# Kernel tuning notes

Hardware: AMD Instinct MI355X
Metric: run time of the kernel (lower is better)

The kernel has to match this reference:

```python
import jax, jax.numpy as jnp
import numpy as np

B, N_COLS, N_PROMPTS, D = 1024, 256, 128, 256


def _ln(x, g, b, eps=1e-5):
    m = jnp.mean(x, axis=-1, keepdims=True)
    v = jnp.mean(jnp.square(x - m), axis=-1, keepdims=True)
    return (x - m) * jax.lax.rsqrt(v + eps) * g + b


def setup_inputs() -> dict:
    key = jax.random.key(0)
    ks = jax.random.split(key, 10)
    d_rs = D ** -0.5
    return {
        "x": jax.random.normal(ks[0], (B, N_COLS), jnp.float32),
        "prev_cell_out": jax.random.normal(ks[1], (B, N_PROMPTS, D), jnp.float32),
        "feature_emb_weight": jax.random.uniform(ks[2], (N_COLS, D), jnp.float32, -d_rs, d_rs),
        "feature_emb_bias": jax.random.uniform(ks[3], (N_COLS, D), jnp.float32, -d_rs, d_rs),
        "ln_emb_g": jnp.ones((D,), jnp.float32),
        "ln_emb_b": jnp.zeros((D,), jnp.float32),
        "ln_col_g": jnp.ones((D,), jnp.float32),
        "ln_col_b": jnp.zeros((D,), jnp.float32),
        "ln_prompt_g": jnp.ones((D,), jnp.float32),
        "ln_prompt_b": jnp.zeros((D,), jnp.float32),
        # torch Linear(2*D, D): weight [D, 2*D], y = x @ W^T + b
        "dense_imp_w": jax.random.normal(ks[4], (D, 2 * D), jnp.float32) * (2 * D) ** -0.5,
        "dense_imp_b": jnp.zeros((D,), jnp.float32),
        "emb_column": jax.random.normal(ks[5], (N_COLS, D), jnp.float32) * 0.01,
        "emb_prompt": jax.random.normal(ks[6], (N_PROMPTS, D), jnp.float32) * 0.01,
        # dense_expand = Linear(1, n_prompts): weight [n_prompts,1] squeezed -> [n_prompts]
        "expand_w": jax.random.normal(ks[7], (N_PROMPTS,), jnp.float32),
        "expand_b": jax.random.normal(ks[8], (N_PROMPTS,), jnp.float32) * 0.01,
    }


def reference(x, prev_cell_out, feature_emb_weight, feature_emb_bias,
              ln_emb_g, ln_emb_b, ln_col_g, ln_col_b, ln_prompt_g, ln_prompt_b,
              dense_imp_w, dense_imp_b, emb_column, emb_prompt,
              expand_w, expand_b):
    # feature embedding: [B, N, D]
    x_emb = jax.nn.relu(jnp.einsum('bn,nd->bnd', x, feature_emb_weight) + feature_emb_bias)
    x_emb = _ln(x_emb, ln_emb_g, ln_emb_b)
    # prompt update with residual
    xp = jnp.broadcast_to(emb_prompt[None], (x.shape[0], N_PROMPTS, D))  # [B, P, D]
    cat = jnp.concatenate([_ln(xp, ln_prompt_g, ln_prompt_b), prev_cell_out], axis=-1)  # [B, P, 2D]
    xp = jnp.einsum('bpk,dk->bpd', cat, dense_imp_w) + dense_imp_b + xp
    # column keys (shared across batch)
    col = _ln(emb_column, ln_col_g, ln_col_b)  # [N, D]
    mask = jax.nn.softmax(jnp.einsum('bpd,nd->bpn', xp, col), axis=-1)  # [B, P, N]
    V = jnp.einsum('bpn,bnd->bpd', mask, x_emb)  # [B, P, D]
    return V * (1.0 + expand_w)[None, :, None] + expand_b[None, :, None]
```

## Files before the change

kernel.cpp:

```cpp
#include <hip/hip_runtime.h>

#define NCOLS 256
#define NP    128
#define DD    256

typedef _Float16 half2 __attribute__((ext_vector_type(2)));
typedef _Float16 half4 __attribute__((ext_vector_type(4)));
typedef float    f32x4 __attribute__((ext_vector_type(4)));

#define MFMA16(a,b,c) __builtin_amdgcn_mfma_f32_16x16x16f16(a,b,c,0,0,0)

#define WS_COL_LN   0
#define WS_LNP      262144
#define WS_BASE     393216
#define WS_BLOG     524288
#define WS_CW16     655360
#define WS_WB16     786432

#define LDS_CWP   3072
#define LDS_XE0   68608
#define LDS_XE1   101376
#define SMEM_MAIN 134144


__global__ __launch_bounds__(256) void k0a(
    const float* __restrict__ emb_column, const float* __restrict__ emb_prompt,
    const float* __restrict__ ln_col_g, const float* __restrict__ ln_col_b,
    const float* __restrict__ ln_prompt_g, const float* __restrict__ ln_prompt_b,
    const float* __restrict__ few, const float* __restrict__ feb,
    char* __restrict__ ws)
{
    __shared__ float red[10];
    int blk = blockIdx.x, tid = threadIdx.x;
    if (blk < 384) {
        const float *src, *g, *bb; float* dst;
        if (blk < 256) { int r = blk;     src = emb_column + r*DD; g = ln_col_g;    bb = ln_col_b;    dst = (float*)(ws + WS_COL_LN) + r*DD; }
        else           { int r = blk-256; src = emb_prompt + r*DD; g = ln_prompt_g; bb = ln_prompt_b; dst = (float*)(ws + WS_LNP) + r*DD; }
        float v = src[tid];
        float s = v, q = v*v;
        #pragma unroll
        for (int off = 32; off; off >>= 1) { s += __shfl_xor(s, off); q += __shfl_xor(q, off); }
        int wid = tid >> 6, lane = tid & 63;
        if (lane == 0) { red[wid] = s; red[4+wid] = q; }
        __syncthreads();
        if (tid == 0) {
            float S = red[0]+red[1]+red[2]+red[3];
            float Q = red[4]+red[5]+red[6]+red[7];
            float mu = S * (1.0f/DD);
            float var = Q * (1.0f/DD) - mu*mu;
            red[8] = mu; red[9] = rsqrtf(var + 1e-5f);
        }
        __syncthreads();
        dst[tid] = (v - red[8]) * red[9] * g[tid] + bb[tid];
    } else {
        int base = (blk - 384) * 512;
        half2* wb = (half2*)(ws + WS_WB16);
        #pragma unroll
        for (int j = 0; j < 2; ++j) {
            int idx = base + j*256 + tid;
            half2 h; h[0] = (_Float16)few[idx]; h[1] = (_Float16)feb[idx];
            wb[idx] = h;
        }
    }
}

__global__ __launch_bounds__(256) void k0b(
    const float* __restrict__ diw, const float* __restrict__ dib,
    const float* __restrict__ emb_prompt, char* __restrict__ ws)
{
    __shared__ float rowv[DD];
    int blk = blockIdx.x, tid = threadIdx.x;
    if (blk < 256) {
        int n = blk;
        const float* col_ln = (const float*)(ws + WS_COL_LN);
        rowv[tid] = col_ln[n*DD + tid];
        __syncthreads();
        float acc = 0.f;
        #pragma unroll 4
        for (int d = 0; d < DD; ++d) acc += rowv[d] * diw[d*512 + 256 + tid];
        int nt = n >> 4, lr = n & 15;
        int kc = tid >> 4, lq = (tid >> 2) & 3, j = tid & 3;
        ((_Float16*)(ws + WS_CW16))[((kc*16 + nt)*64 + lq*16 + lr)*4 + j] = (_Float16)acc;
    } else {
        int p = blk - 256;
        const float* lnp = (const float*)(ws + WS_LNP);
        rowv[tid] = lnp[p*DD + tid];
        __syncthreads();
        float acc = 0.f;
        #pragma unroll 4
        for (int k = 0; k < DD; ++k) acc += rowv[k] * diw[tid*512 + k];
        ((float*)(ws + WS_BASE))[p*DD + tid] = acc + dib[tid] + emb_prompt[p*DD + tid];
    }
}

__global__ __launch_bounds__(256) void k0c(char* __restrict__ ws)
{
    __shared__ float bs[DD];
    int p = blockIdx.x, n = threadIdx.x;
    const float* base   = (const float*)(ws + WS_BASE);
    const float* col_ln = (const float*)(ws + WS_COL_LN);
    bs[n] = base[p*DD + n];
    __syncthreads();
    float acc = 0.f;
    #pragma unroll 4
    for (int d = 0; d < DD; ++d) acc += bs[d] * col_ln[n*DD + d];
    ((float*)(ws + WS_BLOG))[p*DD + n] = acc;
}

__global__ __launch_bounds__(1024) void trompt_main(
    const float* __restrict__ x, const float* __restrict__ prev,
    const float* __restrict__ expand_w, const float* __restrict__ expand_b,
    const float* __restrict__ ln_emb_g, const float* __restrict__ ln_emb_b,
    const char* __restrict__ ws, float* __restrict__ out)
{
    extern __shared__ char smem[];
    float* x_s  = (float*)(smem);
    float* sm_m = (float*)(smem + 1024);
    float* sm_l = (float*)(smem + 2048);
    char*  cwP  = smem + LDS_CWP;
    char*  xe0  = smem + LDS_XE0;
    char*  xe1  = smem + LDS_XE1;

    const char*  cwbase = ws + WS_CW16;
    const half2* WB     = (const half2*)(ws + WS_WB16);

    int b = blockIdx.x;
    int tid = threadIdx.x;
    int w = tid >> 6, l = tid & 63, lq = l >> 4, lr = l & 15;
    int pt = w >> 1, h = w & 1;
    int p  = 16*pt + lr;
    int pswz = (p & 7) << 4;

    if (tid < 256) x_s[tid] = x[b*NCOLS + tid];

    #pragma unroll
    for (int i = 0; i < 8; ++i) {
        int u = tid + 1024*i;
        *(uint4*)(cwP + u*16) = *(const uint4*)(cwbase + u*16);
    }

    half4 pfrag[16];
    {
        const float* prow = prev + ((size_t)b*NP + p)*DD + 4*lq;
        #pragma unroll
        for (int kc = 0; kc < 16; ++kc) {
            f32x4 v = *(const f32x4*)(prow + 16*kc);
            half4 hh;
            #pragma unroll
            for (int j = 0; j < 4; ++j) hh[j] = (_Float16)v[j];
            pfrag[kc] = hh;
        }
    }

    f32x4 acc[8];
    {
        const float* blrow = (const float*)(ws + WS_BLOG) + (size_t)p*DD + 4*lq;
        #pragma unroll
        for (int a = 0; a < 8; ++a) acc[a] = *(const f32x4*)(blrow + 16*(8*h + a));
    }

    __syncthreads();

    {
        const char* cwl = cwP + l*8 + (size_t)(8*h)*512;
        #pragma unroll
        for (int kc = 0; kc < 16; ++kc) {
            const char* fb = cwl + (size_t)kc*8192;
            half4 bp = pfrag[kc];
            #pragma unroll
            for (int a = 0; a < 8; ++a)
                acc[a] = MFMA16(*(const half4*)(fb + a*512), bp, acc[a]);
        }
    }

    float pmax = -1e30f;
    #pragma unroll
    for (int a = 0; a < 8; ++a)
        #pragma unroll
        for (int r = 0; r < 4; ++r) pmax = fmaxf(pmax, acc[a][r]);
    pmax = fmaxf(pmax, __shfl_xor(pmax, 16));
    pmax = fmaxf(pmax, __shfl_xor(pmax, 32));
    if (lq == 0) sm_m[h*128 + p] = pmax;
    __syncthreads();
    float m = fmaxf(pmax, sm_m[(1 ^ h)*128 + p]);

    float s = 0.f;
    #pragma unroll
    for (int a = 0; a < 8; ++a)
        #pragma unroll
        for (int r = 0; r < 4; ++r) { float e = __expf(acc[a][r] - m); acc[a][r] = e; s += e; }
    s += __shfl_xor(s, 16);
    s += __shfl_xor(s, 32);
    if (lq == 0) sm_l[h*128 + p] = s;
    __syncthreads();
    float inv = 1.0f / (s + sm_l[(1 ^ h)*128 + p]);

    #pragma unroll
    for (int a = 0; a < 8; ++a) {
        int nb = (8*h + a)*32 + lq*8;
        half4 hh;
        #pragma unroll
        for (int r = 0; r < 4; ++r) hh[r] = (_Float16)(acc[a][r] * inv);
        *(half4*)(cwP + p*512 + (nb ^ pswz)) = hh;
    }

    float gcc[4], bcc[4];
    #pragma unroll
    for (int cc = 0; cc < 4; ++cc) {
        gcc[cc] = ln_emb_g[l + 64*cc];
        bcc[cc] = ln_emb_b[l + 64*cc];
    }

    auto compute_xe = [&](int c, char* xebuf) {
        int kc2w = w >> 2, lq2 = w & 3;
        float vj[4][4];
        #pragma unroll
        for (int j = 0; j < 4; ++j) {
            int n = c*64 + 16*kc2w + 4*lq2 + j;
            float xv = x_s[n];
            const half2* wbrow = WB + n*DD;
            float ss = 0.f, qq = 0.f;
            #pragma unroll
            for (int cc = 0; cc < 4; ++cc) {
                half2 pp = wbrow[l + 64*cc];
                float e = fmaf(xv, (float)pp[0], (float)pp[1]);
                e = e > 0.f ? e : 0.f;
                vj[j][cc] = e; ss += e; qq += e*e;
            }
            #pragma unroll
            for (int off = 32; off; off >>= 1) { ss += __shfl_xor(ss, off); qq += __shfl_xor(qq, off); }
            float mu = ss * (1.0f/DD);
            float rs = rsqrtf(qq*(1.0f/DD) - mu*mu + 1e-5f);
            #pragma unroll
            for (int cc = 0; cc < 4; ++cc)
                vj[j][cc] = (vj[j][cc]-mu)*rs*gcc[cc] + bcc[cc];
        }
        #pragma unroll
        for (int cc = 0; cc < 4; ++cc) {
            int dt = 4*cc + (l >> 4);
            half4 hh;
            #pragma unroll
            for (int j = 0; j < 4; ++j) hh[j] = (_Float16)vj[j][cc];
            *(half4*)(xebuf + (((kc2w*16 + dt)*64) + lq2*16 + lr)*8) = hh;
        }
    };

    compute_xe(0, xe0);

    f32x4 acc_v[8];
    #pragma unroll
    for (int dtl = 0; dtl < 8; ++dtl) acc_v[dtl] = (f32x4){0.f,0.f,0.f,0.f};

    __syncthreads();

    for (int c = 0; c < 4; ++c) {
        char* xec = (c & 1) ? xe1 : xe0;
        char* xen = (c & 1) ? xe0 : xe1;

        half4 bp[4];
        #pragma unroll
        for (int kc2 = 0; kc2 < 4; ++kc2)
            bp[kc2] = *(const half4*)(cwP + p*512 + ((c*128 + kc2*32 + lq*8) ^ pswz));

        if (c < 3) compute_xe(c+1, xen);

        const char* xel = xec + l*8;
        #pragma unroll
        for (int kc2 = 0; kc2 < 4; ++kc2) {
            const char* xb = xel + (size_t)(kc2*16 + 8*h)*512;
            half4 bpc = bp[kc2];
            #pragma unroll
            for (int dtl = 0; dtl < 8; ++dtl)
                acc_v[dtl] = MFMA16(*(const half4*)(xb + dtl*512), bpc, acc_v[dtl]);
        }

        if (c < 3) __syncthreads();
    }

    {
        float sw = 1.0f + expand_w[p];
        float sb = expand_b[p];
        float* orow = out + ((size_t)b*NP + p)*DD + 128*h + 4*lq;
        #pragma unroll
        for (int dtl = 0; dtl < 8; ++dtl) {
            f32x4 v = acc_v[dtl];
            #pragma unroll
            for (int r = 0; r < 4; ++r) v[r] = v[r]*sw + sb;
            *(f32x4*)(orow + 16*dtl) = v;
        }
    }
}

extern "C" void kernel_launch(void* const* d_in, const int* in_sizes, int n_in,
                              void* d_out, int out_size, void* d_ws, size_t ws_size,
                              hipStream_t stream) {
    (void)in_sizes; (void)n_in; (void)out_size; (void)ws_size;
    const float* x           = (const float*)d_in[0];
    const float* prev        = (const float*)d_in[1];
    const float* few         = (const float*)d_in[2];
    const float* feb         = (const float*)d_in[3];
    const float* ln_emb_g    = (const float*)d_in[4];
    const float* ln_emb_b    = (const float*)d_in[5];
    const float* ln_col_g    = (const float*)d_in[6];
    const float* ln_col_b    = (const float*)d_in[7];
    const float* ln_prompt_g = (const float*)d_in[8];
    const float* ln_prompt_b = (const float*)d_in[9];
    const float* diw         = (const float*)d_in[10];
    const float* dib         = (const float*)d_in[11];
    const float* emb_column  = (const float*)d_in[12];
    const float* emb_prompt  = (const float*)d_in[13];
    const float* expand_w    = (const float*)d_in[14];
    const float* expand_b    = (const float*)d_in[15];
    char* ws = (char*)d_ws;
    float* out = (float*)d_out;

    k0a<<<512, 256, 0, stream>>>(emb_column, emb_prompt, ln_col_g, ln_col_b,
                                 ln_prompt_g, ln_prompt_b, few, feb, ws);
    k0b<<<384, 256, 0, stream>>>(diw, dib, emb_prompt, ws);
    k0c<<<128, 256, 0, stream>>>(ws);

    (void)hipFuncSetAttribute(reinterpret_cast<const void*>(trompt_main),
                              hipFuncAttributeMaxDynamicSharedMemorySize, SMEM_MAIN);
    trompt_main<<<1024, 1024, SMEM_MAIN, stream>>>(x, prev, expand_w, expand_b,
                                                   ln_emb_g, ln_emb_b, ws, out);
}
```

Before: 195.5 us.

## Split prompts across two blocks and stream column weights through double-buffered LDS

```diff
diff --git a/kernel.cpp b/kernel.cpp
--- a/kernel.cpp
+++ b/kernel.cpp
@@ -17,10 +17,11 @@
 #define WS_CW16     655360
 #define WS_WB16     786432
 
-#define LDS_CWP   3072
-#define LDS_XE0   68608
-#define LDS_XE1   101376
-#define SMEM_MAIN 134144
+#define LDS_CW0   2048
+#define LDS_CW1   34816
+#define LDS_XEA   34816
+#define LDS_XEB   51200
+#define SMEM_MAIN 67584
 
 
 __global__ __launch_bounds__(256) void k0a(
@@ -107,7 +108,7 @@
     ((float*)(ws + WS_BLOG))[p*DD + n] = acc;
 }
 
-__global__ __launch_bounds__(1024) void trompt_main(
+__global__ __launch_bounds__(512, 4) void trompt_main(
     const float* __restrict__ x, const float* __restrict__ prev,
     const float* __restrict__ expand_w, const float* __restrict__ expand_b,
     const float* __restrict__ ln_emb_g, const float* __restrict__ ln_emb_b,
@@ -116,28 +117,26 @@
     extern __shared__ char smem[];
     float* x_s  = (float*)(smem);
     float* sm_m = (float*)(smem + 1024);
-    float* sm_l = (float*)(smem + 2048);
-    char*  cwP  = smem + LDS_CWP;
-    char*  xe0  = smem + LDS_XE0;
-    char*  xe1  = smem + LDS_XE1;
+    float* sm_l = (float*)(smem + 1536);
+    char*  cw0  = smem + LDS_CW0;
+    char*  cw1  = smem + LDS_CW1;
+    char*  Pb   = smem + LDS_CW0;
+    char*  xeA  = smem + LDS_XEA;
+    char*  xeB  = smem + LDS_XEB;
 
     const char*  cwbase = ws + WS_CW16;
     const half2* WB     = (const half2*)(ws + WS_WB16);
 
-    int b = blockIdx.x;
+    int bid = blockIdx.x;
+    int b = bid >> 1, ph = bid & 1;
     int tid = threadIdx.x;
     int w = tid >> 6, l = tid & 63, lq = l >> 4, lr = l & 15;
     int pt = w >> 1, h = w & 1;
-    int p  = 16*pt + lr;
-    int pswz = (p & 7) << 4;
+    int pl = 16*pt + lr;
+    int p  = 64*ph + pl;
+    int pswz = (pl & 7) << 4;
 
     if (tid < 256) x_s[tid] = x[b*NCOLS + tid];
-
-    #pragma unroll
-    for (int i = 0; i < 8; ++i) {
-        int u = tid + 1024*i;
-        *(uint4*)(cwP + u*16) = *(const uint4*)(cwbase + u*16);
-    }
 
     half4 pfrag[16];
     {
@@ -156,21 +155,57 @@
     {
         const float* blrow = (const float*)(ws + WS_BLOG) + (size_t)p*DD + 4*lq;
         #pragma unroll
-        for (int a = 0; a < 8; ++a) acc[a] = *(const f32x4*)(blrow + 16*(8*h + a));
-    }
-
-    __syncthreads();
-
-    {
-        const char* cwl = cwP + l*8 + (size_t)(8*h)*512;
+        for (int a = 0; a < 8; ++a)
+            acc[a] = *(const f32x4*)(blrow + 16*(4*(a>>1) + 2*h + (a&1)));
+    }
+
+    auto stage_cw = [&](int c, char* dst) {
+        #pragma unroll
+        for (int i = 0; i < 4; ++i) {
+            int u = tid + 512*i;
+            int kc = u >> 7, ntg = (u >> 5) & 3, rem = u & 31;
+            uint4 v = *(const uint4*)(cwbase + kc*8192 + c*2048 + ntg*512 + rem*16);
+            *(uint4*)(dst + u*16) = v;
+        }
+    };
+
+    stage_cw(0, cw0);
+    __syncthreads();
+
+    #pragma unroll
+    for (int c = 0; c < 4; ++c) {
+        char* cwc = (c & 1) ? cw1 : cw0;
+        char* cwn = (c & 1) ? cw0 : cw1;
+
+        uint4 st[4];
+        if (c < 3) {
+            #pragma unroll
+            for (int i = 0; i < 4; ++i) {
+                int u = tid + 512*i;
+                int kc = u >> 7, ntg = (u >> 5) & 3, rem = u & 31;
+                st[i] = *(const uint4*)(cwbase + kc*8192 + (c+1)*2048 + ntg*512 + rem*16);
+            }
+        }
+
+        const char* cwl = cwc + l*8 + h*1024;
         #pragma unroll
         for (int kc = 0; kc < 16; ++kc) {
-            const char* fb = cwl + (size_t)kc*8192;
+            const char* fb = cwl + kc*2048;
+            half4 a0 = *(const half4*)(fb);
+            half4 a1 = *(const half4*)(fb + 512);
             half4 bp = pfrag[kc];
-            #pragma unroll
-            for (int a = 0; a < 8; ++a)
-                acc[a] = MFMA16(*(const half4*)(fb + a*512), bp, acc[a]);
-        }
+            acc[2*c]   = MFMA16(a0, bp, acc[2*c]);
+            acc[2*c+1] = MFMA16(a1, bp, acc[2*c+1]);
+        }
+
+        if (c < 3) {
+            #pragma unroll
+            for (int i = 0; i < 4; ++i) {
+                int u = tid + 512*i;
+                *(uint4*)(cwn + u*16) = st[i];
+            }
+        }
+        __syncthreads();
     }
 
     float pmax = -1e30f;
@@ -180,9 +215,9 @@
         for (int r = 0; r < 4; ++r) pmax = fmaxf(pmax, acc[a][r]);
     pmax = fmaxf(pmax, __shfl_xor(pmax, 16));
     pmax = fmaxf(pmax, __shfl_xor(pmax, 32));
-    if (lq == 0) sm_m[h*128 + p] = pmax;
-    __syncthreads();
-    float m = fmaxf(pmax, sm_m[(1 ^ h)*128 + p]);
+    if (lq == 0) sm_m[h*64 + pl] = pmax;
+    __syncthreads();
+    float m = fmaxf(pmax, sm_m[(1 ^ h)*64 + pl]);
 
     float s = 0.f;
     #pragma unroll
@@ -191,17 +226,17 @@
         for (int r = 0; r < 4; ++r) { float e = __expf(acc[a][r] - m); acc[a][r] = e; s += e; }
     s += __shfl_xor(s, 16);
     s += __shfl_xor(s, 32);
-    if (lq == 0) sm_l[h*128 + p] = s;
-    __syncthreads();
-    float inv = 1.0f / (s + sm_l[(1 ^ h)*128 + p]);
+    if (lq == 0) sm_l[h*64 + pl] = s;
+    __syncthreads();
+    float inv = 1.0f / (s + sm_l[(1 ^ h)*64 + pl]);
 
     #pragma unroll
     for (int a = 0; a < 8; ++a) {
-        int nb = (8*h + a)*32 + lq*8;
+        int nb = (4*(a>>1) + 2*h + (a&1))*32 + lq*8;
         half4 hh;
         #pragma unroll
         for (int r = 0; r < 4; ++r) hh[r] = (_Float16)(acc[a][r] * inv);
-        *(half4*)(cwP + p*512 + (nb ^ pswz)) = hh;
+        *(half4*)(Pb + pl*512 + (nb ^ pswz)) = hh;
     }
 
     float gcc[4], bcc[4];
@@ -211,41 +246,41 @@
         bcc[cc] = ln_emb_b[l + 64*cc];
     }
 
-    auto compute_xe = [&](int c, char* xebuf) {
+    auto compute_xe = [&](int cc, char* xebuf) {
         int kc2w = w >> 2, lq2 = w & 3;
         float vj[4][4];
         #pragma unroll
         for (int j = 0; j < 4; ++j) {
-            int n = c*64 + 16*kc2w + 4*lq2 + j;
+            int n = cc*32 + 16*kc2w + 4*lq2 + j;
             float xv = x_s[n];
             const half2* wbrow = WB + n*DD;
             float ss = 0.f, qq = 0.f;
             #pragma unroll
-            for (int cc = 0; cc < 4; ++cc) {
-                half2 pp = wbrow[l + 64*cc];
+            for (int ccc = 0; ccc < 4; ++ccc) {
+                half2 pp = wbrow[l + 64*ccc];
                 float e = fmaf(xv, (float)pp[0], (float)pp[1]);
                 e = e > 0.f ? e : 0.f;
-                vj[j][cc] = e; ss += e; qq += e*e;
+                vj[j][ccc] = e; ss += e; qq += e*e;
             }
             #pragma unroll
             for (int off = 32; off; off >>= 1) { ss += __shfl_xor(ss, off); qq += __shfl_xor(qq, off); }
             float mu = ss * (1.0f/DD);
             float rs = rsqrtf(qq*(1.0f/DD) - mu*mu + 1e-5f);
             #pragma unroll
-            for (int cc = 0; cc < 4; ++cc)
-                vj[j][cc] = (vj[j][cc]-mu)*rs*gcc[cc] + bcc[cc];
-        }
-        #pragma unroll
-        for (int cc = 0; cc < 4; ++cc) {
-            int dt = 4*cc + (l >> 4);
+            for (int ccc = 0; ccc < 4; ++ccc)
+                vj[j][ccc] = (vj[j][ccc]-mu)*rs*gcc[ccc] + bcc[ccc];
+        }
+        #pragma unroll
+        for (int ccc = 0; ccc < 4; ++ccc) {
+            int dt = 4*ccc + (l >> 4);
             half4 hh;
             #pragma unroll
-            for (int j = 0; j < 4; ++j) hh[j] = (_Float16)vj[j][cc];
+            for (int j = 0; j < 4; ++j) hh[j] = (_Float16)vj[j][ccc];
             *(half4*)(xebuf + (((kc2w*16 + dt)*64) + lq2*16 + lr)*8) = hh;
         }
     };
 
-    compute_xe(0, xe0);
+    compute_xe(0, xeA);
 
     f32x4 acc_v[8];
     #pragma unroll
@@ -253,28 +288,24 @@
 
     __syncthreads();
 
-    for (int c = 0; c < 4; ++c) {
-        char* xec = (c & 1) ? xe1 : xe0;
-        char* xen = (c & 1) ? xe0 : xe1;
-
-        half4 bp[4];
-        #pragma unroll
-        for (int kc2 = 0; kc2 < 4; ++kc2)
-            bp[kc2] = *(const half4*)(cwP + p*512 + ((c*128 + kc2*32 + lq*8) ^ pswz));
-
-        if (c < 3) compute_xe(c+1, xen);
+    for (int cc = 0; cc < 8; ++cc) {
+        char* xec = (cc & 1) ? xeB : xeA;
+        char* xen = (cc & 1) ? xeA : xeB;
+
+        half4 bp0 = *(const half4*)(Pb + pl*512 + ((cc*64 +  0 + lq*8) ^ pswz));
+        half4 bp1 = *(const half4*)(Pb + pl*512 + ((cc*64 + 32 + lq*8) ^ pswz));
+
+        if (cc < 7) compute_xe(cc+1, xen);
 
         const char* xel = xec + l*8;
         #pragma unroll
-        for (int kc2 = 0; kc2 < 4; ++kc2) {
-            const char* xb = xel + (size_t)(kc2*16 + 8*h)*512;
-            half4 bpc = bp[kc2];
-            #pragma unroll
-            for (int dtl = 0; dtl < 8; ++dtl)
-                acc_v[dtl] = MFMA16(*(const half4*)(xb + dtl*512), bpc, acc_v[dtl]);
-        }
-
-        if (c < 3) __syncthreads();
+        for (int dtl = 0; dtl < 8; ++dtl)
+            acc_v[dtl] = MFMA16(*(const half4*)(xel + (size_t)(8*h + dtl)*512), bp0, acc_v[dtl]);
+        #pragma unroll
+        for (int dtl = 0; dtl < 8; ++dtl)
+            acc_v[dtl] = MFMA16(*(const half4*)(xel + (size_t)(16 + 8*h + dtl)*512), bp1, acc_v[dtl]);
+
+        __syncthreads();
     }
 
     {
@@ -321,6 +352,6 @@
 
     (void)hipFuncSetAttribute(reinterpret_cast<const void*>(trompt_main),
                               hipFuncAttributeMaxDynamicSharedMemorySize, SMEM_MAIN);
-    trompt_main<<<1024, 1024, SMEM_MAIN, stream>>>(x, prev, expand_w, expand_b,
-                                                   ln_emb_g, ln_emb_b, ws, out);
-}
+    trompt_main<<<2048, 512, SMEM_MAIN, stream>>>(x, prev, expand_w, expand_b,
+                                                  ln_emb_g, ln_emb_b, ws, out);
+}
```

After: 223.3 us. +14.2%, slower.

## Use 16x16x32 f16 MFMA for logits and merge softmax into one barrier

Applied to the files above, without the earlier changes.

```diff
diff --git a/kernel.cpp b/kernel.cpp
--- a/kernel.cpp
+++ b/kernel.cpp
@@ -6,9 +6,11 @@
 
 typedef _Float16 half2 __attribute__((ext_vector_type(2)));
 typedef _Float16 half4 __attribute__((ext_vector_type(4)));
+typedef _Float16 half8 __attribute__((ext_vector_type(8)));
 typedef float    f32x4 __attribute__((ext_vector_type(4)));
 
 #define MFMA16(a,b,c) __builtin_amdgcn_mfma_f32_16x16x16f16(a,b,c,0,0,0)
+#define MFMA32(a,b,c) __builtin_amdgcn_mfma_f32_16x16x32_f16(a,b,c,0,0,0)
 
 #define WS_COL_LN   0
 #define WS_LNP      262144
@@ -79,8 +81,8 @@
         #pragma unroll 4
         for (int d = 0; d < DD; ++d) acc += rowv[d] * diw[d*512 + 256 + tid];
         int nt = n >> 4, lr = n & 15;
-        int kc = tid >> 4, lq = (tid >> 2) & 3, j = tid & 3;
-        ((_Float16*)(ws + WS_CW16))[((kc*16 + nt)*64 + lq*16 + lr)*4 + j] = (_Float16)acc;
+        int kc32 = tid >> 5, lq = (tid >> 3) & 3, jj = tid & 7;
+        ((_Float16*)(ws + WS_CW16))[(kc32*16 + nt)*512 + (lq*16 + lr)*8 + jj] = (_Float16)acc;
     } else {
         int p = blk - 256;
         const float* lnp = (const float*)(ws + WS_LNP);
@@ -133,74 +135,77 @@
 
     if (tid < 256) x_s[tid] = x[b*NCOLS + tid];
 
+    half8 pf[8];
+    {
+        const float* prow = prev + ((size_t)b*NP + p)*DD + 8*lq;
+        #pragma unroll
+        for (int kc = 0; kc < 8; ++kc) {
+            f32x4 v0 = *(const f32x4*)(prow + 32*kc);
+            f32x4 v1 = *(const f32x4*)(prow + 32*kc + 4);
+            half8 hh;
+            #pragma unroll
+            for (int j = 0; j < 4; ++j) { hh[j] = (_Float16)v0[j]; hh[4+j] = (_Float16)v1[j]; }
+            pf[kc] = hh;
+        }
+    }
+
+    f32x4 acc[8];
+    {
+        const float* blrow = (const float*)(ws + WS_BLOG) + (size_t)p*DD + 4*lq;
+        #pragma unroll
+        for (int a = 0; a < 8; ++a) acc[a] = *(const f32x4*)(blrow + 16*(8*h + a));
+    }
+
     #pragma unroll
     for (int i = 0; i < 8; ++i) {
         int u = tid + 1024*i;
         *(uint4*)(cwP + u*16) = *(const uint4*)(cwbase + u*16);
     }
 
-    half4 pfrag[16];
+    __syncthreads();
+
     {
-        const float* prow = prev + ((size_t)b*NP + p)*DD + 4*lq;
-        #pragma unroll
-        for (int kc = 0; kc < 16; ++kc) {
-            f32x4 v = *(const f32x4*)(prow + 16*kc);
-            half4 hh;
-            #pragma unroll
-            for (int j = 0; j < 4; ++j) hh[j] = (_Float16)v[j];
-            pfrag[kc] = hh;
-        }
-    }
-
-    f32x4 acc[8];
-    {
-        const float* blrow = (const float*)(ws + WS_BLOG) + (size_t)p*DD + 4*lq;
-        #pragma unroll
-        for (int a = 0; a < 8; ++a) acc[a] = *(const f32x4*)(blrow + 16*(8*h + a));
-    }
-
+        const char* cwl = cwP + (size_t)(8*h)*1024 + l*16;
+        #pragma unroll
+        for (int kc = 0; kc < 8; ++kc) {
+            const char* fb = cwl + (size_t)kc*16384;
+            half8 bp = pf[kc];
+            #pragma unroll
+            for (int a = 0; a < 8; ++a)
+                acc[a] = MFMA32(*(const half8*)(fb + a*1024), bp, acc[a]);
+        }
+    }
+
+    float mh = -1e30f;
+    #pragma unroll
+    for (int a = 0; a < 8; ++a)
+        #pragma unroll
+        for (int r = 0; r < 4; ++r) mh = fmaxf(mh, acc[a][r]);
+    mh = fmaxf(mh, __shfl_xor(mh, 16));
+    mh = fmaxf(mh, __shfl_xor(mh, 32));
+
+    float sh = 0.f;
+    #pragma unroll
+    for (int a = 0; a < 8; ++a)
+        #pragma unroll
+        for (int r = 0; r < 4; ++r) { float e = __expf(acc[a][r] - mh); acc[a][r] = e; sh += e; }
+    sh += __shfl_xor(sh, 16);
+    sh += __shfl_xor(sh, 32);
+
+    if (lq == 0) { sm_m[h*128 + p] = mh; sm_l[h*128 + p] = sh; }
     __syncthreads();
-
-    {
-        const char* cwl = cwP + l*8 + (size_t)(8*h)*512;
-        #pragma unroll
-        for (int kc = 0; kc < 16; ++kc) {
-            const char* fb = cwl + (size_t)kc*8192;
-            half4 bp = pfrag[kc];
-            #pragma unroll
-            for (int a = 0; a < 8; ++a)
-                acc[a] = MFMA16(*(const half4*)(fb + a*512), bp, acc[a]);
-        }
-    }
-
-    float pmax = -1e30f;
-    #pragma unroll
-    for (int a = 0; a < 8; ++a)
-        #pragma unroll
-        for (int r = 0; r < 4; ++r) pmax = fmaxf(pmax, acc[a][r]);
-    pmax = fmaxf(pmax, __shfl_xor(pmax, 16));
-    pmax = fmaxf(pmax, __shfl_xor(pmax, 32));
-    if (lq == 0) sm_m[h*128 + p] = pmax;
-    __syncthreads();
-    float m = fmaxf(pmax, sm_m[(1 ^ h)*128 + p]);
-
-    float s = 0.f;
-    #pragma unroll
-    for (int a = 0; a < 8; ++a)
-        #pragma unroll
-        for (int r = 0; r < 4; ++r) { float e = __expf(acc[a][r] - m); acc[a][r] = e; s += e; }
-    s += __shfl_xor(s, 16);
-    s += __shfl_xor(s, 32);
-    if (lq == 0) sm_l[h*128 + p] = s;
-    __syncthreads();
-    float inv = 1.0f / (s + sm_l[(1 ^ h)*128 + p]);
+    float mo = sm_m[(1 ^ h)*128 + p];
+    float so = sm_l[(1 ^ h)*128 + p];
+    float M  = fmaxf(mh, mo);
+    float eh = __expf(mh - M), eo = __expf(mo - M);
+    float fac = eh / (sh*eh + so*eo);
 
     #pragma unroll
     for (int a = 0; a < 8; ++a) {
         int nb = (8*h + a)*32 + lq*8;
         half4 hh;
         #pragma unroll
-        for (int r = 0; r < 4; ++r) hh[r] = (_Float16)(acc[a][r] * inv);
+        for (int r = 0; r < 4; ++r) hh[r] = (_Float16)(acc[a][r] * fac);
         *(half4*)(cwP + p*512 + (nb ^ pswz)) = hh;
     }
 
@@ -211,8 +216,8 @@
         bcc[cc] = ln_emb_b[l + 64*cc];
     }
 
+    int kc2w = w >> 2, lq2 = w & 3;
     auto compute_xe = [&](int c, char* xebuf) {
-        int kc2w = w >> 2, lq2 = w & 3;
         float vj[4][4];
         #pragma unroll
         for (int j = 0; j < 4; ++j) {
```

Result: faster. 185.7 us (-5.0%).
